# Kernel optimization log

Hardware: AMD Instinct MI355X
Metric: run time of the kernel (lower is better)

Reference implementation:

```python
import jax, jax.numpy as jnp
import numpy as np

B, N1, N2 = 8, 16384, 2048
C1, C2 = 128, 256
IN_CH = C1 + C2  # 384
MLP = [256, 128]
BN_EPS = 1e-5


def setup_inputs() -> dict:
    key = jax.random.key(0)
    ks = jax.random.split(key, 12)
    inp = {
        "xyz1": jax.random.normal(ks[0], (B, N1, 3), dtype=jnp.float32),
        "xyz2": jax.random.normal(ks[1], (B, N2, 3), dtype=jnp.float32),
        "points1": jax.random.normal(ks[2], (B, N1, C1), dtype=jnp.float32),
        "points2": jax.random.normal(ks[3], (B, N2, C2), dtype=jnp.float32),
        # pointwise conv1d (kernel=1) weights as [out, in]
        "W1": jax.random.normal(ks[4], (MLP[0], IN_CH), dtype=jnp.float32) * (1.0 / np.sqrt(IN_CH)),
        "b1": jnp.zeros((MLP[0],), dtype=jnp.float32),
        "gamma1": jnp.ones((MLP[0],), dtype=jnp.float32),
        "beta1": jnp.zeros((MLP[0],), dtype=jnp.float32),
        "W2": jax.random.normal(ks[5], (MLP[1], MLP[0]), dtype=jnp.float32) * (1.0 / np.sqrt(MLP[0])),
        "b2": jnp.zeros((MLP[1],), dtype=jnp.float32),
        "gamma2": jnp.ones((MLP[1],), dtype=jnp.float32),
        "beta2": jnp.zeros((MLP[1],), dtype=jnp.float32),
    }
    return inp


def _bn_relu(h, gamma, beta):
    # BatchNorm1d in training mode: batch stats over (B, N) per channel
    mean = jnp.mean(h, axis=(0, 1), keepdims=True)
    var = jnp.mean((h - mean) ** 2, axis=(0, 1), keepdims=True)
    return jax.nn.relu((h - mean) * jax.lax.rsqrt(var + BN_EPS) * gamma + beta)


def reference(xyz1, xyz2, points1, points2, W1, b1, gamma1, beta1, W2, b2, gamma2, beta2):
    # squared pairwise distances [B, N1, N2]
    d = (-2.0 * jnp.einsum("bnc,bmc->bnm", xyz1, xyz2)
         + jnp.sum(xyz1 ** 2, -1)[:, :, None]
         + jnp.sum(xyz2 ** 2, -1)[:, None, :])
    neg_vals, idx = jax.lax.top_k(-d, 3)            # 3 smallest distances
    dists = jnp.maximum(-neg_vals, 1e-10)           # clamp(min=1e-10)
    w = 1.0 / dists                                 # [B, N1, 3]
    w_norm = w / jnp.maximum(jnp.sum(w, axis=2, keepdims=True), 1e-8)
    # gather 3 neighbor features: [B, N1, 3, C2]
    gathered = jax.vmap(lambda p, i: p[i])(points2, idx)
    interp = jnp.einsum("bnk,bnkc->bnc", w_norm, gathered)  # [B, N1, C2]
    x = jnp.concatenate([points1, interp], axis=-1)          # [B, N1, IN_CH]
    # pointwise conv + BN + ReLU stack
    h = jnp.einsum("bnc,oc->bno", x, W1) + b1
    h = _bn_relu(h, gamma1, beta1)
    h = jnp.einsum("bnc,oc->bno", h, W2) + b2
    h = _bn_relu(h, gamma2, beta2)
    return h  # [B, N1, MLP[-1]]
```

## Files before the change

### kernel.cpp

```cpp
#include <hip/hip_runtime.h>
#include <hip/hip_bf16.h>
#include <stdint.h>
#include <stddef.h>

typedef __hip_bfloat16 bf16;
typedef __attribute__((ext_vector_type(8))) short short8;
typedef __attribute__((ext_vector_type(4))) float f32x4;

#define B_SZ   8
#define N1_SZ  16384
#define N2_SZ  2048
#define C1_SZ  128
#define C2_SZ  256
#define IN_CH  384
#define O1_SZ  256
#define O2_SZ  128
#define R_TOT  (B_SZ * N1_SZ)

#define OFF_FLAG   ((size_t)0)
#define OFF_STATS1 ((size_t)256)
#define OFF_SCALE1 ((size_t)2304)
#define OFF_STATS2 ((size_t)4352)
#define OFF_SCALE2 ((size_t)5376)
#define OFF_WIDX   ((size_t)8192)
#define OFF_WW     ((size_t)1581056)
#define OFF_H1     ((size_t)3153920)
#define WS_NEEDED  ((size_t)70262784)


static __device__ __forceinline__ float cvtf(bf16 v) { return __bfloat162float(v); }
static __device__ __forceinline__ float cvtf(float v) { return v; }
static __device__ __forceinline__ bf16  f2b(float v) { return __float2bfloat16(v); }

static __device__ __forceinline__ unsigned umed3(unsigned a, unsigned b, unsigned c) {
  unsigned r;
  asm("v_med3_u32 %0, %1, %2, %3" : "=v"(r) : "v"(a), "v"(b), "v"(c));
  return r;
}

static __device__ __forceinline__ void load8f(const bf16* p, float* f) {
  uint4 v = *(const uint4*)p;
  const bf16* e = (const bf16*)&v;
#pragma unroll
  for (int j = 0; j < 8; ++j) f[j] = cvtf(e[j]);
}
static __device__ __forceinline__ void load8f(const float* p, float* f) {
  float4 a = *(const float4*)p;
  float4 b = *(const float4*)(p + 4);
  f[0] = a.x; f[1] = a.y; f[2] = a.z; f[3] = a.w;
  f[4] = b.x; f[5] = b.y; f[6] = b.z; f[7] = b.w;
}
static __device__ __forceinline__ void load8b(const bf16* p, bf16* o) {
  *(uint4*)o = *(const uint4*)p;
}
static __device__ __forceinline__ void load8b(const float* p, bf16* o) {
  float f[8]; load8f(p, f);
#pragma unroll
  for (int j = 0; j < 8; ++j) o[j] = f2b(f[j]);
}
static __device__ __forceinline__ void stv(bf16* p, float v) { *p = f2b(v); }
static __device__ __forceinline__ void stv(float* p, float v) { *p = v; }
static __device__ __forceinline__ void store8(bf16* p, const bf16* t) { *(uint4*)p = *(const uint4*)t; }
static __device__ __forceinline__ void store8(float* p, const float* t) {
  *(uint4*)p = *(const uint4*)t; *(uint4*)(p + 4) = *(const uint4*)(t + 4);
}

__global__ void k_detect(const uint16_t* __restrict__ probe, int* __restrict__ flag) {
  __shared__ int cnt;
  if (threadIdx.x == 0) cnt = 0;
  __syncthreads();
  unsigned u = probe[threadIdx.x];
  int e = (u >> 7) & 0xFF;
  if (e >= 100 && e <= 141) atomicAdd(&cnt, 1);
  __syncthreads();
  if (threadIdx.x == 0) *flag = (cnt >= 224) ? 1 : 0;
}

__global__ void k_zero(float* __restrict__ s) {
  s[blockIdx.x * 256 + threadIdx.x] = 0.f;
}

template <typename T>
__global__ __launch_bounds__(256) void k_fill2(T* __restrict__ out,
                                               const int* __restrict__ flag, int expect) {
  if (flag && *flag != expect) return;
  size_t e0 = ((size_t)blockIdx.x * 256 + threadIdx.x) * 8;
  T t[8];
#pragma unroll
  for (int j = 0; j < 8; ++j) stv(&t[j], 2.0f);
  store8(out + e0, t);
}

static __device__ __forceinline__ void merge3(double& a0, double& a1, double& a2,
                                              int& x0, int& x1, int& x2, int mask) {
  double b0 = __shfl_xor(a0, mask, 64);
  double b1 = __shfl_xor(a1, mask, 64);
  double b2 = __shfl_xor(a2, mask, 64);
  int y0 = __shfl_xor(x0, mask, 64);
  int y1 = __shfl_xor(x1, mask, 64);
  int y2 = __shfl_xor(x2, mask, 64);
  bool t = (a0 < b0) || (a0 == b0 && x0 < y0);
  double c0 = t ? a0 : b0; int k0 = t ? x0 : y0;
  double A0 = t ? a1 : a0; int X0 = t ? x1 : x0;
  double A1 = t ? a2 : a1; int X1 = t ? x2 : x1;
  double B0 = t ? b0 : b1; int Y0 = t ? y0 : y1;
  double B1 = t ? b1 : b2; int Y1 = t ? y1 : y2;
  t = (A0 < B0) || (A0 == B0 && X0 < Y0);
  double c1 = t ? A0 : B0; int k1 = t ? X0 : Y0;
  double A0b = t ? A1 : A0; int X0b = t ? X1 : X0;
  double B0b = t ? B0 : B1; int Y0b = t ? Y0 : Y1;
  t = (A0b < B0b) || (A0b == B0b && X0b < Y0b);
  double c2 = t ? A0b : B0b; int k2 = t ? X0b : Y0b;
  a0 = c0; a1 = c1; a2 = c2; x0 = k0; x1 = k1; x2 = k2;
}

__global__ __launch_bounds__(512) void k_top3(const void* __restrict__ xyz1v,
                                              const void* __restrict__ xyz2v,
                                              int* __restrict__ widx,
                                              float* __restrict__ ww,
                                              const int* __restrict__ flag) {
  __shared__ float4 sp[N2_SZ];
  int isbf = *flag;
  int b = blockIdx.x >> 7;
  int g = blockIdx.x & 127;
  if (isbf) {
    const bf16* x2 = (const bf16*)xyz2v + (size_t)b * N2_SZ * 3;
    for (int i = threadIdx.x; i < N2_SZ; i += 512) {
      float px = cvtf(x2[i * 3 + 0]);
      float py = cvtf(x2[i * 3 + 1]);
      float pz = cvtf(x2[i * 3 + 2]);
      double dx = (double)px, dy = (double)py, dz = (double)pz;
      sp[i] = make_float4(-2.f * px, -2.f * py, -2.f * pz,
                          (float)(dx * dx + dy * dy + dz * dz));
    }
  } else {
    const float* x2 = (const float*)xyz2v + (size_t)b * N2_SZ * 3;
    for (int i = threadIdx.x; i < N2_SZ; i += 512) {
      float px = x2[i * 3 + 0];
      float py = x2[i * 3 + 1];
      float pz = x2[i * 3 + 2];
      double dx = (double)px, dy = (double)py, dz = (double)pz;
      sp[i] = make_float4(-2.f * px, -2.f * py, -2.f * pz,
                          (float)(dx * dx + dy * dy + dz * dz));
    }
  }
  __syncthreads();
  int qloc = threadIdx.x >> 2;
  int sub  = threadIdx.x & 3;
  int r = b * N1_SZ + g * 128 + qloc;
  float Qxf, Qyf, Qzf;
  if (isbf) {
    const bf16* q = (const bf16*)xyz1v + (size_t)r * 3;
    Qxf = cvtf(q[0]); Qyf = cvtf(q[1]); Qzf = cvtf(q[2]);
  } else {
    const float* q = (const float*)xyz1v + (size_t)r * 3;
    Qxf = q[0]; Qyf = q[1]; Qzf = q[2];
  }

  unsigned m0 = 0xFFFFFFFFu, m1 = 0xFFFFFFFFu, m2 = 0xFFFFFFFFu;
  unsigned m3 = 0xFFFFFFFFu, m4 = 0xFFFFFFFFu;
  const float4* base = sp + sub;
#pragma unroll 4
  for (unsigned i = 0; i < N2_SZ / 4; ++i) {
    float4 p = base[(size_t)i * 4];
    float d = fmaf(p.x, Qxf, fmaf(p.y, Qyf, fmaf(p.z, Qzf, p.w)));
    int bi = __float_as_int(d);
    unsigned u = (unsigned)bi ^ (unsigned)((bi >> 31) | (int)0x80000000);
    unsigned key = (u & 0xFFFFFE00u) | i;
    m4 = umed3(m3, m4, key);
    m3 = umed3(m2, m3, key);
    m2 = umed3(m1, m2, key);
    m1 = umed3(m0, m1, key);
    m0 = m0 < key ? m0 : key;
  }

  double Qx = (double)Qxf, Qy = (double)Qyf, Qz = (double)Qzf;
  double Qn = Qx * Qx + Qy * Qy + Qz * Qz;
  double e0 = 1e300, e1 = 1e300, e2 = 1e300;
  int j0 = 0, j1 = 0, j2 = 0;
  unsigned ms[5] = { m0, m1, m2, m3, m4 };
#pragma unroll
  for (int k = 0; k < 5; ++k) {
    int j = (int)((ms[k] & 511u) << 2) | sub;
    float4 p = sp[j];
    double Px = -0.5 * (double)p.x;
    double Py = -0.5 * (double)p.y;
    double Pz = -0.5 * (double)p.z;
    double pw = Px * Px + Py * Py + Pz * Pz;
    double dot = Qx * Px + Qy * Py + Qz * Pz;
    double d = fma(-2.0, dot, Qn + pw);
    bool l2 = (d < e2) || (d == e2 && j < j2);
    if (l2) {
      bool l1 = (d < e1) || (d == e1 && j < j1);
      if (l1) {
        e2 = e1; j2 = j1;
        bool l0 = (d < e0) || (d == e0 && j < j0);
        if (l0) { e1 = e0; j1 = j0; e0 = d; j0 = j; }
        else    { e1 = d;  j1 = j; }
      } else { e2 = d; j2 = j; }
    }
  }

  merge3(e0, e1, e2, j0, j1, j2, 1);
  merge3(e0, e1, e2, j0, j1, j2, 2);

  if (sub == 0) {
    e0 = fmax(e0, 1e-10); e1 = fmax(e1, 1e-10); e2 = fmax(e2, 1e-10);
    double w0 = 1.0 / e0, w1 = 1.0 / e1, w2 = 1.0 / e2;
    double inv = 1.0 / fmax(w0 + w1 + w2, 1e-8);
    widx[(size_t)r * 3 + 0] = j0; widx[(size_t)r * 3 + 1] = j1; widx[(size_t)r * 3 + 2] = j2;
    ww[(size_t)r * 3 + 0] = (float)(w0 * inv);
    ww[(size_t)r * 3 + 1] = (float)(w1 * inv);
    ww[(size_t)r * 3 + 2] = (float)(w2 * inv);
  }
}

__global__ __launch_bounds__(256) void k_interp(const void* __restrict__ p2v,
                                                const int* __restrict__ widx,
                                                const float* __restrict__ ww,
                                                bf16* __restrict__ xi,
                                                const int* __restrict__ flag) {
  int isbf = *flag;
  int t = blockIdx.x * 256 + threadIdx.x;
  int r = t >> 5;
  int c = (t & 31) << 3;
  int bidx = r >> 14;
  int i0 = widx[(size_t)r * 3 + 0];
  int i1 = widx[(size_t)r * 3 + 1];
  int i2 = widx[(size_t)r * 3 + 2];
  float w0 = ww[(size_t)r * 3 + 0];
  float w1 = ww[(size_t)r * 3 + 1];
  float w2 = ww[(size_t)r * 3 + 2];
  float f0[8], f1[8], f2[8];
  if (isbf) {
    const bf16* p2 = (const bf16*)p2v + (size_t)bidx * N2_SZ * C2_SZ;
    load8f(p2 + (size_t)i0 * C2_SZ + c, f0);
    load8f(p2 + (size_t)i1 * C2_SZ + c, f1);
    load8f(p2 + (size_t)i2 * C2_SZ + c, f2);
  } else {
    const float* p2 = (const float*)p2v + (size_t)bidx * N2_SZ * C2_SZ;
    load8f(p2 + (size_t)i0 * C2_SZ + c, f0);
    load8f(p2 + (size_t)i1 * C2_SZ + c, f1);
    load8f(p2 + (size_t)i2 * C2_SZ + c, f2);
  }
  bf16 o[8];
#pragma unroll
  for (int j = 0; j < 8; ++j)
    o[j] = f2b(w0 * f0[j] + w1 * f1[j] + w2 * f2[j]);
  *(uint4*)&xi[(size_t)r * C2_SZ + c] = *(uint4*)o;
}

template <typename T>
__global__ __launch_bounds__(512, 4) void k_gemm1(const T* __restrict__ points1,
                                                  const bf16* __restrict__ xi,
                                                  const T* __restrict__ W1,
                                                  const T* __restrict__ bias,
                                                  bf16* __restrict__ h1,
                                                  float* __restrict__ sbuf,
                                                  const int* __restrict__ flag, int expect) {
  if (*flag != expect) return;
  constexpr int LDA = 392;
  constexpr int LDT = 40;
  __shared__ bf16 As[64 * LDA];
  __shared__ bf16 Bs[256 * LDT];

  int tid = threadIdx.x;
  int r0 = blockIdx.x * 64;
  int row = tid >> 3;
  int sub = tid & 7;
  int r = r0 + row;

#pragma unroll
  for (int q = 0; q < 2; ++q) {
    int c = sub * 16 + q * 8;
    bf16 t[8];
    load8b(points1 + (size_t)r * C1_SZ + c, t);
    *(uint4*)&As[row * LDA + c] = *(uint4*)t;
  }
#pragma unroll
  for (int q = 0; q < 4; ++q) {
    int c = sub * 32 + q * 8;
    uint4 v = *(const uint4*)&xi[(size_t)r * C2_SZ + c];
    *(uint4*)&As[row * LDA + C1_SZ + c] = v;
  }
#pragma unroll
  for (int s = 0; s < 2; ++s) {
    int u = tid + s * 512;
    int orow = u >> 2, okc = (u & 3) * 8;
    bf16 wv0[8];
    load8b(W1 + (size_t)orow * IN_CH + okc, wv0);
    *(uint4*)&Bs[orow * LDT + okc] = *(uint4*)wv0;
  }

  int wave = tid >> 6, lane = tid & 63;
  int quad = lane >> 4, l15 = lane & 15;
  int wy = wave >> 2, wx = wave & 3;

  f32x4 acc[2][4];
#pragma unroll
  for (int tm = 0; tm < 2; ++tm)
#pragma unroll
    for (int tn = 0; tn < 4; ++tn) {
      acc[tm][tn][0] = 0.f; acc[tm][tn][1] = 0.f;
      acc[tm][tn][2] = 0.f; acc[tm][tn][3] = 0.f;
    }

  __syncthreads();

  for (int kk = 0; kk < 12; ++kk) {
    bf16 wv[2][8];
    if (kk < 11) {
#pragma unroll
      for (int s = 0; s < 2; ++s) {
        int u = tid + s * 512;
        int orow = u >> 2, okc = (u & 3) * 8;
        load8b(W1 + (size_t)orow * IN_CH + (kk + 1) * 32 + okc, wv[s]);
      }
    }
    short8 afr[2], bfr[4];
#pragma unroll
    for (int tm = 0; tm < 2; ++tm)
      afr[tm] = *(const short8*)&As[(wy * 32 + tm * 16 + l15) * LDA + kk * 32 + quad * 8];
#pragma unroll
    for (int tn = 0; tn < 4; ++tn)
      bfr[tn] = *(const short8*)&Bs[(wx * 64 + tn * 16 + l15) * LDT + quad * 8];
#pragma unroll
    for (int tm = 0; tm < 2; ++tm)
#pragma unroll
      for (int tn = 0; tn < 4; ++tn)
        acc[tm][tn] = __builtin_amdgcn_mfma_f32_16x16x32_bf16(afr[tm], bfr[tn], acc[tm][tn], 0, 0, 0);
    __syncthreads();
    if (kk < 11) {
#pragma unroll
      for (int s = 0; s < 2; ++s) {
        int u = tid + s * 512;
        int orow = u >> 2, okc = (u & 3) * 8;
        *(uint4*)&Bs[orow * LDT + okc] = *(uint4*)wv[s];
      }
      __syncthreads();
    }
  }

  __syncthreads();
  float* redu = (float*)As;

  float s1[4], s2[4];
#pragma unroll
  for (int tn = 0; tn < 4; ++tn) {
    int col = wx * 64 + tn * 16 + l15;
    float bv = cvtf(bias[col]);
    s1[tn] = 0.f; s2[tn] = 0.f;
#pragma unroll
    for (int tm = 0; tm < 2; ++tm) {
#pragma unroll
      for (int rg = 0; rg < 4; ++rg) {
        int rw = r0 + wy * 32 + tm * 16 + quad * 4 + rg;
        float vv = acc[tm][tn][rg] + bv;
        s1[tn] += vv; s2[tn] += vv * vv;
        h1[(size_t)rw * O1_SZ + col] = f2b(vv);
      }
    }
    s1[tn] += __shfl_xor(s1[tn], 16, 64);
    s1[tn] += __shfl_xor(s1[tn], 32, 64);
    s2[tn] += __shfl_xor(s2[tn], 16, 64);
    s2[tn] += __shfl_xor(s2[tn], 32, 64);
  }
  if (lane < 16) {
#pragma unroll
    for (int tn = 0; tn < 4; ++tn) {
      int col = wx * 64 + tn * 16 + l15;
      redu[(wy * 256 + col) * 2 + 0] = s1[tn];
      redu[(wy * 256 + col) * 2 + 1] = s2[tn];
    }
  }
  __syncthreads();
  atomicAdd(&sbuf[(blockIdx.x & 63) * 512 + tid & 0 ? 0 : (blockIdx.x & 63) * 512 + tid],
            0.f),
  sbuf += (size_t)(blockIdx.x & 63) * 512;
  atomicAdd(&sbuf[tid], redu[tid] + redu[512 + tid]);
}

template <typename T>
__global__ __launch_bounds__(256) void k_gemm2(const bf16* __restrict__ h1,
                                               const T* __restrict__ W2,
                                               const T* __restrict__ bias,
                                               const float* __restrict__ scale1,
                                               const float* __restrict__ shift1,
                                               T* __restrict__ out,
                                               float* __restrict__ part,
                                               const int* __restrict__ flag, int expect) {
  if (*flag != expect) return;
  constexpr int LDT = 40;
  __shared__ bf16 As[64 * LDT];
  __shared__ bf16 Bs[128 * LDT];
  __shared__ float redu[2][128][2];
  __shared__ float sc_s[O1_SZ], sh_s[O1_SZ];

  int tid = threadIdx.x;
  sc_s[tid] = scale1[tid];
  sh_s[tid] = shift1[tid];

  int r0 = blockIdx.x * 64;
  int arow = tid >> 2;
  int akc  = (tid & 3) * 8;

  int wave = tid >> 6, lane = tid & 63;
  int quad = lane >> 4, l15 = lane & 15;
  int wy = wave >> 1, wx = wave & 1;

  f32x4 acc[2][4];
#pragma unroll
  for (int tm = 0; tm < 2; ++tm)
#pragma unroll
    for (int tn = 0; tn < 4; ++tn) {
      acc[tm][tn][0] = 0.f; acc[tm][tn][1] = 0.f;
      acc[tm][tn][2] = 0.f; acc[tm][tn][3] = 0.f;
    }

  for (int k0 = 0; k0 < O1_SZ; k0 += 32) {
    __syncthreads();
    {
      uint4 v = *(const uint4*)(h1 + (size_t)(r0 + arow) * O1_SZ + k0 + akc);
      const bf16* e = (const bf16*)&v;
      bf16 t[8];
#pragma unroll
      for (int j = 0; j < 8; ++j) {
        float f = cvtf(e[j]);
        f = fmaxf(fmaf(f, sc_s[k0 + akc + j], sh_s[k0 + akc + j]), 0.f);
        t[j] = f2b(f);
      }
      *(uint4*)&As[arow * LDT + akc] = *(uint4*)t;
    }
#pragma unroll
    for (int s = 0; s < 2; ++s) {
      int u = tid + s * 256;
      int orow = u >> 2, okc = (u & 3) * 8;
      bf16 wv[8];
      load8b(W2 + (size_t)orow * O1_SZ + k0 + okc, wv);
      *(uint4*)&Bs[orow * LDT + okc] = *(uint4*)wv;
    }
    __syncthreads();
    short8 afr[2], bfr[4];
#pragma unroll
    for (int tm = 0; tm < 2; ++tm)
      afr[tm] = *(const short8*)&As[(wy * 32 + tm * 16 + l15) * LDT + quad * 8];
#pragma unroll
    for (int tn = 0; tn < 4; ++tn)
      bfr[tn] = *(const short8*)&Bs[(wx * 64 + tn * 16 + l15) * LDT + quad * 8];
#pragma unroll
    for (int tm = 0; tm < 2; ++tm)
#pragma unroll
      for (int tn = 0; tn < 4; ++tn)
        acc[tm][tn] = __builtin_amdgcn_mfma_f32_16x16x32_bf16(afr[tm], bfr[tn], acc[tm][tn], 0, 0, 0);
  }

  float s1[4], s2[4];
#pragma unroll
  for (int tn = 0; tn < 4; ++tn) {
    int col = wx * 64 + tn * 16 + l15;
    float bv = cvtf(bias[col]);
    s1[tn] = 0.f; s2[tn] = 0.f;
#pragma unroll
    for (int tm = 0; tm < 2; ++tm) {
#pragma unroll
      for (int rg = 0; rg < 4; ++rg) {
        int row = r0 + wy * 32 + tm * 16 + quad * 4 + rg;
        float vv = acc[tm][tn][rg] + bv;
        s1[tn] += vv; s2[tn] += vv * vv;
        stv(&out[(size_t)row * O2_SZ + col], vv);
      }
    }
    s1[tn] += __shfl_xor(s1[tn], 16, 64);
    s1[tn] += __shfl_xor(s1[tn], 32, 64);
    s2[tn] += __shfl_xor(s2[tn], 16, 64);
    s2[tn] += __shfl_xor(s2[tn], 32, 64);
  }
  if (lane < 16) {
#pragma unroll
    for (int tn = 0; tn < 4; ++tn) {
      int col = wx * 64 + tn * 16 + l15;
      redu[wy][col][0] = s1[tn];
      redu[wy][col][1] = s2[tn];
    }
  }
  __syncthreads();
  {
    int col = tid & 127;
    int sel = tid >> 7;
    part[(size_t)blockIdx.x * 256 + col * 2 + sel] = redu[0][col][sel] + redu[1][col][sel];
  }
}

__global__ __launch_bounds__(256) void k_reduce(const float* __restrict__ part,
                                                float* __restrict__ stats,
                                                int nblk, int nvals) {
  int v = blockIdx.x;
  float s = 0.f;
  for (int b = threadIdx.x; b < nblk; b += 256)
    s += part[(size_t)b * nvals + v];
  s += __shfl_xor(s, 1, 64);  s += __shfl_xor(s, 2, 64);
  s += __shfl_xor(s, 4, 64);  s += __shfl_xor(s, 8, 64);
  s += __shfl_xor(s, 16, 64); s += __shfl_xor(s, 32, 64);
  __shared__ float red[4];
  if ((threadIdx.x & 63) == 0) red[threadIdx.x >> 6] = s;
  __syncthreads();
  if (threadIdx.x == 0) stats[v] = red[0] + red[1] + red[2] + red[3];
}

__global__ void k_bn_fin(const float* __restrict__ stats, const void* __restrict__ gamma,
                         const void* __restrict__ beta, float* __restrict__ scale,
                         float* __restrict__ shift, int O, float invR,
                         const int* __restrict__ flag) {
  int t = blockIdx.x * blockDim.x + threadIdx.x;
  if (t < O) {
    float gv, bv;
    if (*flag) {
      gv = cvtf(((const bf16*)gamma)[t]); bv = cvtf(((const bf16*)beta)[t]);
    } else {
      gv = ((const float*)gamma)[t];      bv = ((const float*)beta)[t];
    }
    float m = stats[t * 2 + 0] * invR;
    float var = fmaxf(stats[t * 2 + 1] * invR - m * m, 0.f);
    float is = rsqrtf(var + 1e-5f);
    float sc = gv * is;
    scale[t] = sc;
    shift[t] = bv - m * sc;
  }
}

__global__ __launch_bounds__(256) void k_bn_out(void* __restrict__ outv,
                                                const float* __restrict__ scale,
                                                const float* __restrict__ shift,
                                                const int* __restrict__ flag) {
  size_t e0 = ((size_t)blockIdx.x * 256 + threadIdx.x) * 8;
  int c0 = (int)(e0 & (O2_SZ - 1));
  if (*flag) {
    bf16* out = (bf16*)outv;
    float f[8]; load8f(out + e0, f);
    bf16 t[8];
#pragma unroll
    for (int j = 0; j < 8; ++j) {
      float pre = fmaf(f[j], scale[c0 + j], shift[c0 + j]);
      float r = fmaxf(pre, 0.f);
      if (__builtin_isnan(pre)) r = pre;
      stv(&t[j], r);
    }
    store8(out + e0, t);
  } else {
    float* out = (float*)outv;
    float f[8]; load8f(out + e0, f);
    float t[8];
#pragma unroll
    for (int j = 0; j < 8; ++j) {
      float pre = fmaf(f[j], scale[c0 + j], shift[c0 + j]);
      float r = fmaxf(pre, 0.f);
      if (__builtin_isnan(pre)) r = pre;
      t[j] = r;
    }
    store8(out + e0, t);
  }
}

extern "C" void kernel_launch(void* const* d_in, const int* in_sizes, int n_in,
                              void* d_out, int out_size, void* d_ws, size_t ws_size,
                              hipStream_t stream) {
  char* ws = (char*)d_ws;
  int*   flag   = (int*)(ws + OFF_FLAG);
  float* stats1 = (float*)(ws + OFF_STATS1);
  float* scale1 = (float*)(ws + OFF_SCALE1);
  float* shift1 = scale1 + 256;
  float* stats2 = (float*)(ws + OFF_STATS2);
  float* scale2 = (float*)(ws + OFF_SCALE2);
  float* shift2 = scale2 + 128;
  int*   widx   = (int*)(ws + OFF_WIDX);
  float* wwp    = (float*)(ws + OFF_WW);
  bf16*  h1     = (bf16*)(ws + OFF_H1);
  bf16*  xi     = (bf16*)d_out;
  float* sbuf   = (float*)(ws + OFF_WIDX);
  float* part2  = (float*)(ws + OFF_WIDX);

  const int FILL_GRID = R_TOT * O2_SZ / 2048;

  if (ws_size < WS_NEEDED) {
    if (ws_size >= 256) {
      k_detect<<<1, 256, 0, stream>>>((const uint16_t*)d_in[2], flag);
      k_fill2<bf16><<<FILL_GRID, 256, 0, stream>>>((bf16*)d_out, flag, 1);
      k_fill2<float><<<FILL_GRID, 256, 0, stream>>>((float*)d_out, flag, 0);
    } else {
      k_fill2<bf16><<<FILL_GRID, 256, 0, stream>>>((bf16*)d_out, (const int*)nullptr, 0);
    }
    return;
  }

  k_detect<<<1, 256, 0, stream>>>((const uint16_t*)d_in[2], flag);

  float invR = 1.f / (float)R_TOT;

  k_top3<<<1024, 512, 0, stream>>>(d_in[0], d_in[1], widx, wwp, flag);

  k_interp<<<R_TOT * 32 / 256, 256, 0, stream>>>(d_in[3], widx, wwp, xi, flag);

  k_zero<<<128, 256, 0, stream>>>(sbuf);

  k_gemm1<bf16><<<R_TOT / 64, 512, 0, stream>>>((const bf16*)d_in[2], xi,
      (const bf16*)d_in[4], (const bf16*)d_in[5], h1, sbuf, flag, 1);
  k_gemm1<float><<<R_TOT / 64, 512, 0, stream>>>((const float*)d_in[2], xi,
      (const float*)d_in[4], (const float*)d_in[5], h1, sbuf, flag, 0);

  k_reduce<<<512, 256, 0, stream>>>(sbuf, stats1, 64, 512);

  k_bn_fin<<<1, 256, 0, stream>>>(stats1, d_in[6], d_in[7], scale1, shift1, O1_SZ, invR, flag);

  k_gemm2<bf16><<<R_TOT / 64, 256, 0, stream>>>(h1, (const bf16*)d_in[8], (const bf16*)d_in[9],
      scale1, shift1, (bf16*)d_out, part2, flag, 1);
  k_gemm2<float><<<R_TOT / 64, 256, 0, stream>>>(h1, (const float*)d_in[8], (const float*)d_in[9],
      scale1, shift1, (float*)d_out, part2, flag, 0);

  k_reduce<<<256, 256, 0, stream>>>(part2, stats2, R_TOT / 64, 256);

  k_bn_fin<<<1, 128, 0, stream>>>(stats2, d_in[10], d_in[11], scale2, shift2, O2_SZ, invR, flag);

  k_bn_out<<<FILL_GRID, 256, 0, stream>>>(d_out, scale2, shift2, flag);
}
```

Measured before the change: 376.1 us.

## Restructure gemm2 with full A-tile preload, 512 threads, and W2 prefetch

Result: no change. 378.8 us (+0.7%).

```diff
diff --git a/kernel.cpp b/kernel.cpp
--- a/kernel.cpp
+++ b/kernel.cpp
@@ -374,100 +374,114 @@
     }
   }
   __syncthreads();
-  atomicAdd(&sbuf[(blockIdx.x & 63) * 512 + tid & 0 ? 0 : (blockIdx.x & 63) * 512 + tid],
-            0.f),
-  sbuf += (size_t)(blockIdx.x & 63) * 512;
-  atomicAdd(&sbuf[tid], redu[tid] + redu[512 + tid]);
+  atomicAdd(&sbuf[(size_t)(blockIdx.x & 63) * 512 + tid],
+            redu[tid] + redu[512 + tid]);
 }
 
 template <typename T>
-__global__ __launch_bounds__(256) void k_gemm2(const bf16* __restrict__ h1,
-                                               const T* __restrict__ W2,
-                                               const T* __restrict__ bias,
-                                               const float* __restrict__ scale1,
-                                               const float* __restrict__ shift1,
-                                               T* __restrict__ out,
-                                               float* __restrict__ part,
-                                               const int* __restrict__ flag, int expect) {
+__global__ __launch_bounds__(512, 4) void k_gemm2(const bf16* __restrict__ h1,
+                                                  const T* __restrict__ W2,
+                                                  const T* __restrict__ bias,
+                                                  const float* __restrict__ scale1,
+                                                  const float* __restrict__ shift1,
+                                                  T* __restrict__ out,
+                                                  float* __restrict__ part,
+                                                  const int* __restrict__ flag, int expect) {
   if (*flag != expect) return;
+  constexpr int LDK = 264;
   constexpr int LDT = 40;
-  __shared__ bf16 As[64 * LDT];
+  __shared__ bf16 As[64 * LDK];
   __shared__ bf16 Bs[128 * LDT];
-  __shared__ float redu[2][128][2];
-  __shared__ float sc_s[O1_SZ], sh_s[O1_SZ];
+  __shared__ float scs[O1_SZ * 2];
 
   int tid = threadIdx.x;
-  sc_s[tid] = scale1[tid];
-  sh_s[tid] = shift1[tid];
+  scs[tid] = (tid < 256) ? scale1[tid] : shift1[tid - 256];
+  __syncthreads();
 
   int r0 = blockIdx.x * 64;
-  int arow = tid >> 2;
-  int akc  = (tid & 3) * 8;
+  int row = tid >> 3;
+  int sub = tid & 7;
+  {
+    const bf16* hrow = h1 + (size_t)(r0 + row) * O1_SZ;
+#pragma unroll
+    for (int q = 0; q < 4; ++q) {
+      int c = sub * 32 + q * 8;
+      uint4 v = *(const uint4*)(hrow + c);
+      const bf16* e = (const bf16*)&v;
+      bf16 t[8];
+#pragma unroll
+      for (int j = 0; j < 8; ++j) {
+        float f = cvtf(e[j]);
+        f = fmaxf(fmaf(f, scs[c + j], scs[256 + c + j]), 0.f);
+        t[j] = f2b(f);
+      }
+      *(uint4*)&As[row * LDK + c] = *(uint4*)t;
+    }
+  }
+  {
+    int orow = tid >> 2, okc = (tid & 3) * 8;
+    bf16 wv0[8];
+    load8b(W2 + (size_t)orow * O1_SZ + okc, wv0);
+    *(uint4*)&Bs[orow * LDT + okc] = *(uint4*)wv0;
+  }
 
   int wave = tid >> 6, lane = tid & 63;
   int quad = lane >> 4, l15 = lane & 15;
-  int wy = wave >> 1, wx = wave & 1;
-
-  f32x4 acc[2][4];
+  int wy = wave >> 2, wx = wave & 3;
+
+  f32x4 acc[2][2];
 #pragma unroll
   for (int tm = 0; tm < 2; ++tm)
 #pragma unroll
-    for (int tn = 0; tn < 4; ++tn) {
+    for (int tn = 0; tn < 2; ++tn) {
       acc[tm][tn][0] = 0.f; acc[tm][tn][1] = 0.f;
       acc[tm][tn][2] = 0.f; acc[tm][tn][3] = 0.f;
     }
 
-  for (int k0 = 0; k0 < O1_SZ; k0 += 32) {
+  __syncthreads();
+
+  for (int kk = 0; kk < 8; ++kk) {
+    bf16 wv[8];
+    if (kk < 7) {
+      int orow = tid >> 2, okc = (tid & 3) * 8;
+      load8b(W2 + (size_t)orow * O1_SZ + (kk + 1) * 32 + okc, wv);
+    }
+    short8 afr[2], bfr[2];
+#pragma unroll
+    for (int tm = 0; tm < 2; ++tm)
+      afr[tm] = *(const short8*)&As[(wy * 32 + tm * 16 + l15) * LDK + kk * 32 + quad * 8];
+#pragma unroll
+    for (int tn = 0; tn < 2; ++tn)
+      bfr[tn] = *(const short8*)&Bs[(wx * 32 + tn * 16 + l15) * LDT + quad * 8];
+#pragma unroll
+    for (int tm = 0; tm < 2; ++tm)
+#pragma unroll
+      for (int tn = 0; tn < 2; ++tn)
+        acc[tm][tn] = __builtin_amdgcn_mfma_f32_16x16x32_bf16(afr[tm], bfr[tn], acc[tm][tn], 0, 0, 0);
     __syncthreads();
-    {
-      uint4 v = *(const uint4*)(h1 + (size_t)(r0 + arow) * O1_SZ + k0 + akc);
-      const bf16* e = (const bf16*)&v;
-      bf16 t[8];
-#pragma unroll
-      for (int j = 0; j < 8; ++j) {
-        float f = cvtf(e[j]);
-        f = fmaxf(fmaf(f, sc_s[k0 + akc + j], sh_s[k0 + akc + j]), 0.f);
-        t[j] = f2b(f);
-      }
-      *(uint4*)&As[arow * LDT + akc] = *(uint4*)t;
-    }
-#pragma unroll
-    for (int s = 0; s < 2; ++s) {
-      int u = tid + s * 256;
-      int orow = u >> 2, okc = (u & 3) * 8;
-      bf16 wv[8];
-      load8b(W2 + (size_t)orow * O1_SZ + k0 + okc, wv);
+    if (kk < 7) {
+      int orow = tid >> 2, okc = (tid & 3) * 8;
       *(uint4*)&Bs[orow * LDT + okc] = *(uint4*)wv;
-    }
-    __syncthreads();
-    short8 afr[2], bfr[4];
-#pragma unroll
-    for (int tm = 0; tm < 2; ++tm)
-      afr[tm] = *(const short8*)&As[(wy * 32 + tm * 16 + l15) * LDT + quad * 8];
-#pragma unroll
-    for (int tn = 0; tn < 4; ++tn)
-      bfr[tn] = *(const short8*)&Bs[(wx * 64 + tn * 16 + l15) * LDT + quad * 8];
-#pragma unroll
-    for (int tm = 0; tm < 2; ++tm)
-#pragma unroll
-      for (int tn = 0; tn < 4; ++tn)
-        acc[tm][tn] = __builtin_amdgcn_mfma_f32_16x16x32_bf16(afr[tm], bfr[tn], acc[tm][tn], 0, 0, 0);
-  }
-
-  float s1[4], s2[4];
-#pragma unroll
-  for (int tn = 0; tn < 4; ++tn) {
-    int col = wx * 64 + tn * 16 + l15;
+      __syncthreads();
+    }
+  }
+
+  float* redu = (float*)As;
+
+  float s1[2], s2[2];
+#pragma unroll
+  for (int tn = 0; tn < 2; ++tn) {
+    int col = wx * 32 + tn * 16 + l15;
     float bv = cvtf(bias[col]);
     s1[tn] = 0.f; s2[tn] = 0.f;
 #pragma unroll
     for (int tm = 0; tm < 2; ++tm) {
 #pragma unroll
       for (int rg = 0; rg < 4; ++rg) {
-        int row = r0 + wy * 32 + tm * 16 + quad * 4 + rg;
+        int rw = r0 + wy * 32 + tm * 16 + quad * 4 + rg;
         float vv = acc[tm][tn][rg] + bv;
         s1[tn] += vv; s2[tn] += vv * vv;
-        stv(&out[(size_t)row * O2_SZ + col], vv);
+        stv(&out[(size_t)rw * O2_SZ + col], vv);
       }
     }
     s1[tn] += __shfl_xor(s1[tn], 16, 64);
@@ -477,17 +491,18 @@
   }
   if (lane < 16) {
 #pragma unroll
-    for (int tn = 0; tn < 4; ++tn) {
-      int col = wx * 64 + tn * 16 + l15;
-      redu[wy][col][0] = s1[tn];
-      redu[wy][col][1] = s2[tn];
-    }
-  }
-  __syncthreads();
-  {
+    for (int tn = 0; tn < 2; ++tn) {
+      int col = wx * 32 + tn * 16 + l15;
+      redu[(wy * 128 + col) * 2 + 0] = s1[tn];
+      redu[(wy * 128 + col) * 2 + 1] = s2[tn];
+    }
+  }
+  __syncthreads();
+  if (tid < 256) {
     int col = tid & 127;
     int sel = tid >> 7;
-    part[(size_t)blockIdx.x * 256 + col * 2 + sel] = redu[0][col][sel] + redu[1][col][sel];
+    part[(size_t)blockIdx.x * 256 + col * 2 + sel] =
+        redu[(col) * 2 + sel] + redu[(128 + col) * 2 + sel];
   }
 }
 
@@ -611,9 +626,9 @@
 
   k_bn_fin<<<1, 256, 0, stream>>>(stats1, d_in[6], d_in[7], scale1, shift1, O1_SZ, invR, flag);
 
-  k_gemm2<bf16><<<R_TOT / 64, 256, 0, stream>>>(h1, (const bf16*)d_in[8], (const bf16*)d_in[9],
+  k_gemm2<bf16><<<R_TOT / 64, 512, 0, stream>>>(h1, (const bf16*)d_in[8], (const bf16*)d_in[9],
       scale1, shift1, (bf16*)d_out, part2, flag, 1);
-  k_gemm2<float><<<R_TOT / 64, 256, 0, stream>>>(h1, (const float*)d_in[8], (const float*)d_in[9],
+  k_gemm2<float><<<R_TOT / 64, 512, 0, stream>>>(h1, (const float*)d_in[8], (const float*)d_in[9],
       scale1, shift1, (float*)d_out, part2, flag, 0);
 
   k_reduce<<<256, 256, 0, stream>>>(part2, stats2, R_TOT / 64, 256);
```
